# Kernel tuning notes

Measured on AMD Instinct MI355X. Metric: run time of the kernel, lower is better.

The kernel has to match this reference:

```python
import jax, jax.numpy as jnp
import numpy as np

B, N, CIN, COUT, R, K = 8, 4096, 64, 128, 32, 3
GROUPS = 8
GN_EPS = 1e-5


def setup_inputs() -> dict:
    key = jax.random.key(0)
    ks = jax.random.split(key, 6)
    w = lambda k, shape, fan: jax.random.normal(k, shape, jnp.float32) / np.sqrt(fan)
    return dict(
        features=jax.random.normal(ks[0], (B, CIN, N), jnp.float32),
        coords=jax.random.uniform(ks[1], (B, N, 3), jnp.float32),
        conv1_w=w(ks[2], (COUT, CIN, K, K, K), CIN * K ** 3), conv1_b=jnp.zeros((COUT,), jnp.float32),
        gn1_g=jnp.ones((COUT,), jnp.float32), gn1_b=jnp.zeros((COUT,), jnp.float32),
        conv2_w=w(ks[3], (COUT, COUT, K, K, K), COUT * K ** 3), conv2_b=jnp.zeros((COUT,), jnp.float32),
        gn2_g=jnp.ones((COUT,), jnp.float32), gn2_b=jnp.zeros((COUT,), jnp.float32),
        pt_w=w(ks[4], (COUT, CIN), CIN), pt_b=jnp.zeros((COUT,), jnp.float32),
        ptgn_g=jnp.ones((COUT,), jnp.float32), ptgn_b=jnp.zeros((COUT,), jnp.float32),
    )


def swish(x):
    return x * jax.nn.sigmoid(x)


def group_norm(x, gamma, beta):
    # x: [B, C, *spatial]
    b, c = x.shape[0], x.shape[1]
    sp = x.shape[2:]
    xg = x.reshape(b, GROUPS, -1)
    m = xg.mean(-1, keepdims=True)
    v = xg.var(-1, keepdims=True)
    xg = (xg - m) * jax.lax.rsqrt(v + GN_EPS)
    x = xg.reshape(b, c, *sp)
    shape = (1, c) + (1,) * len(sp)
    return x * gamma.reshape(shape) + beta.reshape(shape)


def conv3d(x, w, bias):
    p = K // 2
    y = jax.lax.conv_general_dilated(
        x, w, window_strides=(1, 1, 1), padding=[(p, p)] * 3,
        dimension_numbers=('NCDHW', 'OIDHW', 'NCDHW'))
    return y + bias[None, :, None, None, None]


def voxelize(features, coords):
    # PVCNN avg_voxelize: normalize coords to [0, R-1], round, scatter-mean.
    c = coords - coords.mean(axis=1, keepdims=True)          # [B,N,3]
    scale = 2.0 * jnp.linalg.norm(c, axis=-1).max(axis=1)     # [B], eps=0
    norm_coords = c / scale[:, None, None] + 0.5
    norm_coords = jnp.clip(norm_coords * R, 0.0, R - 1)       # float coords in [0, R-1]
    vox = jnp.round(norm_coords).astype(jnp.int32)
    flat = (vox[..., 0] * R + vox[..., 1]) * R + vox[..., 2]  # [B,N]
    seg = (flat + jnp.arange(B, dtype=jnp.int32)[:, None] * R ** 3).reshape(-1)
    ft = features.transpose(0, 2, 1).reshape(B * N, CIN)
    sums = jax.ops.segment_sum(ft, seg, num_segments=B * R ** 3)
    cnt = jax.ops.segment_sum(jnp.ones((B * N,), ft.dtype), seg, num_segments=B * R ** 3)
    grid = sums / jnp.maximum(cnt, 1.0)[:, None]
    grid = grid.reshape(B, R ** 3, CIN).transpose(0, 2, 1).reshape(B, CIN, R, R, R)
    return grid, norm_coords


def trilinear_devoxelize(grid, norm_coords):
    # grid: [B, C, R, R, R]; norm_coords: [B, N, 3] float in [0, R-1]
    c = grid.shape[1]
    f = jnp.floor(norm_coords)
    d = norm_coords - f                                       # frac, [B,N,3]
    f0 = f.astype(jnp.int32)
    f1 = jnp.minimum(f0 + 1, R - 1)
    gridf = grid.reshape(B, c, R ** 3)
    out = jnp.zeros((B, c, N), grid.dtype)
    for ix in (0, 1):
        for iy in (0, 1):
            for iz in (0, 1):
                xi = f1[..., 0] if ix else f0[..., 0]
                yi = f1[..., 1] if iy else f0[..., 1]
                zi = f1[..., 2] if iz else f0[..., 2]
                wx = d[..., 0] if ix else 1.0 - d[..., 0]
                wy = d[..., 1] if iy else 1.0 - d[..., 1]
                wz = d[..., 2] if iz else 1.0 - d[..., 2]
                idx = (xi * R + yi) * R + zi                  # [B,N]
                g = jnp.take_along_axis(gridf, idx[:, None, :], axis=2)  # [B,C,N]
                out = out + g * (wx * wy * wz)[:, None, :]
    return out


def reference(features, coords, conv1_w, conv1_b, gn1_g, gn1_b,
              conv2_w, conv2_b, gn2_g, gn2_b, pt_w, pt_b, ptgn_g, ptgn_b):
    grid, norm_coords = voxelize(features, coords)
    h = swish(group_norm(conv3d(grid, conv1_w, conv1_b), gn1_g, gn1_b))
    h = swish(group_norm(conv3d(h, conv2_w, conv2_b), gn2_g, gn2_b))
    devox = trilinear_devoxelize(h, norm_coords)              # [B, COUT, N]
    pf = jnp.einsum('oc,bcn->bon', pt_w, features) + pt_b[None, :, None]
    pf = swish(group_norm(pf, ptgn_g, ptgn_b))
    return devox + pf
```

## Files before the change

kernel.cpp:

```cpp
#include <hip/hip_runtime.h>
#include <hip/hip_bf16.h>
#include <cstdint>

#define B_ 8
#define N_ 4096
#define CIN_ 64
#define COUT_ 128
#define R_ 32
#define R3_ 32768
#define GROUPS_ 8
#define EPS_ 1e-5f

typedef float f32x4 __attribute__((ext_vector_type(4)));
typedef float f32x16 __attribute__((ext_vector_type(16)));
typedef __bf16 bf16x8 __attribute__((ext_vector_type(8)));
typedef unsigned short ushort8x __attribute__((ext_vector_type(8)));

static __device__ __forceinline__ unsigned short f2b(float f) {
    uint32_t u = __float_as_uint(f);
    uint32_t r = (u + 0x7fffu + ((u >> 16) & 1u)) >> 16;
    return (unsigned short)r;
}
static __device__ __forceinline__ float b2f(unsigned short u) {
    return __uint_as_float(((uint32_t)u) << 16);
}

__global__ void k_batch_stats(const float* __restrict__ coords, float* __restrict__ bstats) {
    int b = blockIdx.x;
    int tid = threadIdx.x;
    __shared__ float rb[256];
    __shared__ float smean[3];
    const float* cb = coords + (size_t)b * N_ * 3;
    float sx = 0.f, sy = 0.f, sz = 0.f;
    for (int n = tid; n < N_; n += 256) {
        sx += cb[n * 3 + 0];
        sy += cb[n * 3 + 1];
        sz += cb[n * 3 + 2];
    }
    float vals[3] = {sx, sy, sz};
    for (int k = 0; k < 3; ++k) {
        rb[tid] = vals[k];
        __syncthreads();
        for (int s = 128; s > 0; s >>= 1) {
            if (tid < s) rb[tid] += rb[tid + s];
            __syncthreads();
        }
        if (tid == 0) smean[k] = rb[0] / (float)N_;
        __syncthreads();
    }
    float mx = smean[0], my = smean[1], mz = smean[2];
    float m2 = 0.f;
    for (int n = tid; n < N_; n += 256) {
        float dx = cb[n * 3 + 0] - mx, dy = cb[n * 3 + 1] - my, dz = cb[n * 3 + 2] - mz;
        m2 = fmaxf(m2, dx * dx + dy * dy + dz * dz);
    }
    rb[tid] = m2;
    __syncthreads();
    for (int s = 128; s > 0; s >>= 1) {
        if (tid < s) rb[tid] = fmaxf(rb[tid], rb[tid + s]);
        __syncthreads();
    }
    if (tid == 0) {
        bstats[b * 4 + 0] = mx;
        bstats[b * 4 + 1] = my;
        bstats[b * 4 + 2] = mz;
        bstats[b * 4 + 3] = 2.0f * sqrtf(rb[0]);
    }
}

__global__ void k_points(const float* __restrict__ coords, const float* __restrict__ bstats,
                         float* __restrict__ ncoords, int* __restrict__ flatidx,
                         float* __restrict__ cnt) {
    int idx = blockIdx.x * 256 + threadIdx.x;
    int b = idx >> 12, n = idx & (N_ - 1);
    float scale = bstats[b * 4 + 3];
    int vi[3];
    for (int k = 0; k < 3; ++k) {
        float c = coords[((size_t)b * N_ + n) * 3 + k] - bstats[b * 4 + k];
        float nc = fminf(fmaxf((c / scale + 0.5f) * (float)R_, 0.0f), (float)(R_ - 1));
        ncoords[((size_t)b * N_ + n) * 3 + k] = nc;
        vi[k] = (int)rintf(nc);
    }
    int flat = (vi[0] * R_ + vi[1]) * R_ + vi[2];
    flatidx[idx] = flat;
    atomicAdd(&cnt[(size_t)b * R3_ + flat], 1.0f);
}

__global__ void k_scatter(const float* __restrict__ feat, const int* __restrict__ flatidx,
                          float* __restrict__ vox, int b0) {
    int bid = blockIdx.x;
    int nch = bid & 15, ci = (bid >> 4) & 63, bl = bid >> 10;
    int b = b0 + bl;
    int n = nch * 256 + threadIdx.x;
    float v = feat[((size_t)b * CIN_ + ci) * N_ + n];
    int flat = flatidx[b * N_ + n];
    atomicAdd(&vox[((size_t)bl * R3_ + flat) * CIN_ + ci], v);
}

__global__ void k_divide(const float* __restrict__ vox, const float* __restrict__ cnt,
                         unsigned short* __restrict__ gA, int b0) {
    size_t idx8 = (size_t)blockIdx.x * 256 + threadIdx.x;
    size_t voxel = idx8 >> 3;
    float c = cnt[(size_t)b0 * R3_ + voxel];
    float s = 1.0f / fmaxf(c, 1.0f);
    const float4* v4 = (const float4*)vox;
    float4 a = v4[idx8 * 2], b = v4[idx8 * 2 + 1];
    ushort8x o;
    o[0] = f2b(a.x * s); o[1] = f2b(a.y * s); o[2] = f2b(a.z * s); o[3] = f2b(a.w * s);
    o[4] = f2b(b.x * s); o[5] = f2b(b.y * s); o[6] = f2b(b.z * s); o[7] = f2b(b.w * s);
    ((ushort8x*)gA)[idx8] = o;
}

__global__ void k_feat2b(const float* __restrict__ f, unsigned short* __restrict__ fb, int b0) {
    size_t i8 = (size_t)blockIdx.x * 256 + threadIdx.x;
    const float4* s = (const float4*)(f + (size_t)b0 * CIN_ * N_);
    float4 a = s[i8 * 2], b = s[i8 * 2 + 1];
    ushort8x o;
    o[0] = f2b(a.x); o[1] = f2b(a.y); o[2] = f2b(a.z); o[3] = f2b(a.w);
    o[4] = f2b(b.x); o[5] = f2b(b.y); o[6] = f2b(b.z); o[7] = f2b(b.w);
    ((ushort8x*)fb)[i8] = o;
}

__global__ void k_wpack16(const float* __restrict__ w, unsigned short* __restrict__ wp,
                          int Cin, int taps) {
    int e = blockIdx.x * 256 + threadIdx.x;
    int total = taps * Cin * 128;
    if (e >= total) return;
    int KC = Cin / 32;
    int j = e & 7;
    int l = (e >> 3) & 63;
    int rest = e >> 9;
    int ct = rest & 7;
    int stepk = rest >> 3;
    int kc = stepk % KC;
    int t = stepk / KC;
    int co = ct * 16 + (l & 15);
    int ci = kc * 32 + (l >> 4) * 8 + j;
    wp[e] = f2b(w[((size_t)co * Cin + ci) * taps + t]);
}

__global__ void k_wpack32(const float* __restrict__ w, unsigned short* __restrict__ wp,
                          int Cin, int taps) {
    int e = blockIdx.x * 256 + threadIdx.x;
    int total = taps * Cin * 128;
    if (e >= total) return;
    int K16C = Cin / 16;
    int j = e & 7;
    int l = (e >> 3) & 63;
    int nt = (e >> 9) & 3;
    int sk = e >> 11;
    int k16 = sk % K16C;
    int t = sk / K16C;
    int co = nt * 32 + (l & 31);
    int ci = k16 * 16 + (l >> 5) * 8 + j;
    wp[e] = f2b(w[((size_t)co * Cin + ci) * taps + t]);
}

template <int CIN, bool FUSEGN>
__global__ __launch_bounds__(256) void k_conv32(
    const unsigned short* __restrict__ in, const unsigned short* __restrict__ wp,
    const float* __restrict__ bias, const float* __restrict__ instats,
    const float* __restrict__ ingamma, const float* __restrict__ inbeta,
    unsigned short* __restrict__ out, float* __restrict__ stats, int b0) {
    constexpr int K16C = CIN / 16;
    constexpr int S = CIN + 8;
    __shared__ unsigned short abuf[6 * 34 * S];
    __shared__ float s_sum[8], s_sq[8];
    __shared__ float sA[128], sB[128];
    int tid = threadIdx.x;
    int bid = blockIdx.x;
    int yg = bid & 7, x = (bid >> 3) & 31, bl = bid >> 8;
    int y0 = yg * 4;
    int lane = tid & 63, wv = tid >> 6;
    int yp = wv & 1, ch = wv >> 1;
    int col = lane & 31, kh = lane >> 5;

    if (tid < 8) { s_sum[tid] = 0.f; s_sq[tid] = 0.f; }
    if (FUSEGN && tid < 128) {
        int b = b0 + bl;
        int grp = tid >> 4;
        const float ic = 1.0f / (16.0f * R3_);
        float mean = instats[(b * 8 + grp) * 2 + 0] * ic;
        float var = instats[(b * 8 + grp) * 2 + 1] * ic - mean * mean;
        float inv = rsqrtf(var + EPS_);
        float A = ingamma[tid] * inv;
        sA[tid] = A;
        sB[tid] = inbeta[tid] - mean * A;
    }
    for (int i = tid; i < 6 * 2 * (CIN / 8); i += 256) {
        int cy = i / (2 * (CIN / 8));
        int r = i - cy * (2 * (CIN / 8));
        int hz = (r >= (CIN / 8)) ? 33 : 0;
        int c8 = r % (CIN / 8);
        ushort8x zz = {0, 0, 0, 0, 0, 0, 0, 0};
        *(ushort8x*)&abuf[(cy * 34 + hz) * S + c8 * 8] = zz;
    }

    float bv[2];
#pragma unroll
    for (int ntl = 0; ntl < 2; ++ntl) bv[ntl] = bias[ch * 64 + ntl * 32 + col];
    f32x16 acc[2][2];
#pragma unroll
    for (int my = 0; my < 2; ++my)
#pragma unroll
        for (int ntl = 0; ntl < 2; ++ntl)
#pragma unroll
            for (int r = 0; r < 16; ++r) acc[my][ntl][r] = bv[ntl];

    for (int xxi = 0; xxi < 3; ++xxi) {
        int xx = x + xxi - 1;
        if (xx < 0 || xx >= 32) continue;
        __syncthreads();
        for (int i = tid; i < 6 * 32 * (CIN / 8); i += 256) {
            int cy = i / (32 * (CIN / 8));
            int r = i - cy * (32 * (CIN / 8));
            int z = r / (CIN / 8), c8 = r - z * (CIN / 8);
            int yy = y0 - 1 + cy;
            ushort8x v = {0, 0, 0, 0, 0, 0, 0, 0};
            if (yy >= 0 && yy < 32) {
                v = *(const ushort8x*)&in[((size_t)bl * R3_ + xx * 1024 + yy * 32 + z) * CIN + c8 * 8];
                if (FUSEGN) {
#pragma unroll
                    for (int k = 0; k < 8; ++k) {
                        float xv = b2f(v[k]);
                        float s = sA[c8 * 8 + k] * xv + sB[c8 * 8 + k];
                        v[k] = f2b(s / (1.0f + expf(-s)));
                    }
                }
            }
            *(ushort8x*)&abuf[(cy * 34 + z + 1) * S + c8 * 8] = v;
        }
        __syncthreads();

        for (int dy = 0; dy < 3; ++dy) {
            for (int dz = 0; dz < 3; ++dz) {
                int t = (xxi * 3 + dy) * 3 + dz;
#pragma unroll
                for (int k16 = 0; k16 < K16C; ++k16) {
                    const unsigned short* wbase =
                        wp + ((size_t)((t * K16C + k16) * 4 + ch * 2) * 64 + lane) * 8;
                    bf16x8 b0f = *(const bf16x8*)wbase;
                    bf16x8 b1f = *(const bf16x8*)(wbase + 512);
#pragma unroll
                    for (int my = 0; my < 2; ++my) {
                        int cy = yp * 2 + my + dy;
                        bf16x8 a = *(const bf16x8*)
                            &abuf[(cy * 34 + col + dz) * S + k16 * 16 + kh * 8];
                        acc[my][0] = __builtin_amdgcn_mfma_f32_32x32x16_bf16(a, b0f, acc[my][0], 0, 0, 0);
                        acc[my][1] = __builtin_amdgcn_mfma_f32_32x32x16_bf16(a, b1f, acc[my][1], 0, 0, 0);
                    }
                }
            }
        }
    }

    float lsum[2] = {0.f, 0.f}, lsq[2] = {0.f, 0.f};
#pragma unroll
    for (int my = 0; my < 2; ++my) {
        int y = y0 + yp * 2 + my;
#pragma unroll
        for (int ntl = 0; ntl < 2; ++ntl) {
            int co = ch * 64 + ntl * 32 + col;
            unsigned short* op = out + ((size_t)bl * R3_ + x * 1024 + y * 32) * 128 + co;
#pragma unroll
            for (int r = 0; r < 16; ++r) {
                int z = (r & 3) + 8 * (r >> 2) + 4 * kh;
                float vv = acc[my][ntl][r];
                op[(size_t)z * 128] = f2b(vv);
                lsum[ntl] += vv;
                lsq[ntl] += vv * vv;
            }
        }
    }
#pragma unroll
    for (int ntl = 0; ntl < 2; ++ntl) {
        float s = lsum[ntl], q = lsq[ntl];
        s += __shfl_xor(s, 32); q += __shfl_xor(q, 32);
        s += __shfl_xor(s, 1);  q += __shfl_xor(q, 1);
        s += __shfl_xor(s, 2);  q += __shfl_xor(q, 2);
        s += __shfl_xor(s, 4);  q += __shfl_xor(q, 4);
        s += __shfl_xor(s, 8);  q += __shfl_xor(q, 8);
        if (lane == 0 || lane == 16) {
            int g = ch * 4 + ntl * 2 + (col >> 4);
            atomicAdd(&s_sum[g], s);
            atomicAdd(&s_sq[g], q);
        }
    }
    __syncthreads();
    if (tid < 8) {
        int b = b0 + bl;
        atomicAdd(&stats[((size_t)b * 8 + tid) * 2 + 0], s_sum[tid]);
        atomicAdd(&stats[((size_t)b * 8 + tid) * 2 + 1], s_sq[tid]);
    }
}

__global__ __launch_bounds__(256) void k_point_mfma(
    const unsigned short* __restrict__ featb, const unsigned short* __restrict__ wp,
    const float* __restrict__ bias, unsigned short* __restrict__ pf,
    float* __restrict__ stats, int b0) {
    __shared__ __align__(16) unsigned short ALds[256 * 72];
    int tid = threadIdx.x;
    int bid = blockIdx.x;
    int bl = bid >> 4;
    int n0 = (bid & 15) * 256;
    int b = b0 + bl;
    int lane = tid & 63, wv = tid >> 6;
    int nh = wv & 1, ch = wv >> 1;
    int mrow = lane & 15, quad = lane >> 4;

    {
        int c0 = (tid >> 5) * 8;
        int nl = tid & 31;
        for (int u = 0; u < 8; ++u) {
            int n = u * 32 + nl;
            ushort8x v;
#pragma unroll
            for (int k = 0; k < 8; ++k)
                v[k] = featb[((size_t)(bl * 64 + c0 + k)) * N_ + n0 + n];
            *(ushort8x*)&ALds[n * 72 + c0] = v;
        }
    }

    bf16x8 bfr[2][4];
#pragma unroll
    for (int kc = 0; kc < 2; ++kc)
#pragma unroll
        for (int ct = 0; ct < 4; ++ct)
            bfr[kc][ct] = *(const bf16x8*)&wp[((size_t)((kc * 8) + ch * 4 + ct) * 64 + lane) * 8];

    float bv[4];
#pragma unroll
    for (int ct = 0; ct < 4; ++ct) bv[ct] = bias[ch * 64 + ct * 16 + mrow];
    f32x4 acc[8][4];
#pragma unroll
    for (int mt = 0; mt < 8; ++mt)
#pragma unroll
        for (int ct = 0; ct < 4; ++ct) {
            acc[mt][ct][0] = bv[ct]; acc[mt][ct][1] = bv[ct];
            acc[mt][ct][2] = bv[ct]; acc[mt][ct][3] = bv[ct];
        }

    __syncthreads();
#pragma unroll
    for (int kc = 0; kc < 2; ++kc) {
#pragma unroll
        for (int mt = 0; mt < 8; ++mt) {
            bf16x8 a = *(const bf16x8*)
                &ALds[(nh * 128 + mt * 16 + mrow) * 72 + kc * 32 + quad * 8];
#pragma unroll
            for (int ct = 0; ct < 4; ++ct)
                acc[mt][ct] = __builtin_amdgcn_mfma_f32_16x16x32_bf16(
                    a, bfr[kc][ct], acc[mt][ct], 0, 0, 0);
        }
    }

#pragma unroll
    for (int ct = 0; ct < 4; ++ct) {
        int co = ch * 64 + ct * 16 + mrow;
        float s = 0.f, q = 0.f;
#pragma unroll
        for (int mt = 0; mt < 8; ++mt) {
#pragma unroll
            for (int r = 0; r < 4; ++r) {
                int n = nh * 128 + mt * 16 + quad * 4 + r;
                float vv = acc[mt][ct][r];
                pf[((size_t)bl * N_ + n0 + n) * 128 + co] = f2b(vv);
                s += vv;
                q += vv * vv;
            }
        }
#pragma unroll
        for (int off = 32; off >= 1; off >>= 1) {
            s += __shfl_xor(s, off);
            q += __shfl_xor(q, off);
        }
        if (lane == 0) {
            int g = ch * 4 + ct;
            atomicAdd(&stats[((size_t)b * 8 + g) * 2 + 0], s);
            atomicAdd(&stats[((size_t)b * 8 + g) * 2 + 1], q);
        }
    }
}

__global__ __launch_bounds__(256) void k_final(
    const unsigned short* __restrict__ grid, const float* __restrict__ ncoords,
    const unsigned short* __restrict__ pf,
    const float* __restrict__ stats2, const float* __restrict__ g2g,
    const float* __restrict__ g2b,
    const float* __restrict__ statsPt, const float* __restrict__ pgg,
    const float* __restrict__ pgb,
    float* __restrict__ out, int b0) {
    __shared__ int sidx[32][8];
    __shared__ float swt[32][8];
    __shared__ float devt[32 * 129];
    int bid = blockIdx.x;
    int bl = bid >> 7;
    int b = b0 + bl;
    int n0 = (bid & 127) * 32;
    int tid = threadIdx.x;
    if (tid < 32) {
        int n = n0 + tid;
        const float* nc = ncoords + ((size_t)b * N_ + n) * 3;
        float fc[3] = {nc[0], nc[1], nc[2]};
        int i0[3], i1[3];
        float dd[3];
        for (int k = 0; k < 3; ++k) {
            float fl = floorf(fc[k]);
            i0[k] = (int)fl;
            i1[k] = min(i0[k] + 1, R_ - 1);
            dd[k] = fc[k] - fl;
        }
#pragma unroll
        for (int k = 0; k < 8; ++k) {
            int ix = (k >> 2) & 1, iy = (k >> 1) & 1, iz = k & 1;
            int xi = ix ? i1[0] : i0[0];
            int yi = iy ? i1[1] : i0[1];
            int zi = iz ? i1[2] : i0[2];
            sidx[tid][k] = (xi * R_ + yi) * R_ + zi;
            float wx = ix ? dd[0] : 1.0f - dd[0];
            float wy = iy ? dd[1] : 1.0f - dd[1];
            float wz = iz ? dd[2] : 1.0f - dd[2];
            swt[tid][k] = wx * wy * wz;
        }
    }
    __syncthreads();
    int co = tid & 127, pg = tid >> 7;
    int grp = co >> 4;
    const float ic2 = 1.0f / (16.0f * R3_);
    float mean2 = stats2[(b * 8 + grp) * 2 + 0] * ic2;
    float var2 = stats2[(b * 8 + grp) * 2 + 1] * ic2 - mean2 * mean2;
    float inv2 = rsqrtf(var2 + EPS_);
    float A2 = g2g[co] * inv2, B2 = g2b[co] - mean2 * A2;
    const float icp = 1.0f / (16.0f * N_);
    float meanp = statsPt[(b * 8 + grp) * 2 + 0] * icp;
    float varp = statsPt[(b * 8 + grp) * 2 + 1] * icp - meanp * meanp;
    float invp = rsqrtf(varp + EPS_);
    float Ap = pgg[co] * invp, Bp = pgb[co] - meanp * Ap;

    const unsigned short* gp = grid + (size_t)bl * R3_ * 128 + co;
    for (int p = pg; p < 32; p += 2) {
        float acc = 0.f;
#pragma unroll
        for (int k = 0; k < 8; ++k) {
            float s = A2 * b2f(gp[(size_t)sidx[p][k] * 128]) + B2;
            acc += swt[p][k] * (s / (1.0f + expf(-s)));
        }
        float xv = b2f(pf[((size_t)bl * N_ + n0 + p) * 128 + co]);
        float s = Ap * xv + Bp;
        devt[p * 129 + co] = acc + s / (1.0f + expf(-s));
    }
    __syncthreads();
    int pp = tid & 31, cg = tid >> 5;
    float* op = out + (size_t)b * 128 * N_ + n0 + pp;
    for (int c = cg * 16; c < cg * 16 + 16; ++c)
        op[(size_t)c * N_] = devt[pp * 129 + c];
}

extern "C" void kernel_launch(void* const* d_in, const int* in_sizes, int n_in,
                              void* d_out, int out_size, void* d_ws, size_t ws_size,
                              hipStream_t stream) {
    const float* features = (const float*)d_in[0];
    const float* coords = (const float*)d_in[1];
    const float* c1w = (const float*)d_in[2];
    const float* c1b = (const float*)d_in[3];
    const float* g1g = (const float*)d_in[4];
    const float* g1b = (const float*)d_in[5];
    const float* c2w = (const float*)d_in[6];
    const float* c2b = (const float*)d_in[7];
    const float* g2g = (const float*)d_in[8];
    const float* g2b = (const float*)d_in[9];
    const float* ptw = (const float*)d_in[10];
    const float* ptb = (const float*)d_in[11];
    const float* pgg = (const float*)d_in[12];
    const float* pgb = (const float*)d_in[13];
    float* outp = (float*)d_out;

    size_t globals = ((size_t)B_ * R3_ * 4 + 255 & ~(size_t)255)
                   + ((size_t)B_ * N_ * 3 * 4 + 255 & ~(size_t)255)
                   + ((size_t)B_ * N_ * 4 + 255 & ~(size_t)255)
                   + 256 + 2048
                   + ((size_t)27 * 64 * 128 * 2 + 255 & ~(size_t)255)
                   + ((size_t)27 * 128 * 128 * 2 + 255 & ~(size_t)255)
                   + ((size_t)64 * 128 * 2 + 255 & ~(size_t)255)
                   + 8192;
    int CB = 1;
    for (int cb = 8; cb >= 1; cb >>= 1) {
        size_t need = globals
                    + ((size_t)cb * R3_ * 64 * 4)
                    + ((size_t)cb * R3_ * 64 * 2)
                    + ((size_t)cb * R3_ * 128 * 2)
                    + ((size_t)cb * N_ * 128 * 2)
                    + ((size_t)cb * 64 * N_ * 2);
        if (need <= ws_size) { CB = cb; break; }
    }

    char* ws = (char*)d_ws;
    size_t o = 0;
    auto alloc = [&](size_t bytes) {
        size_t r = o;
        o += (bytes + 255) & ~(size_t)255;
        return r;
    };
    float* voxC = (float*)(ws + alloc((size_t)CB * R3_ * 64 * 4));
    unsigned short* gC = (unsigned short*)voxC;
    unsigned short* gA = (unsigned short*)(ws + alloc((size_t)CB * R3_ * 64 * 2));
    unsigned short* gB = (unsigned short*)(ws + alloc((size_t)CB * R3_ * 128 * 2));
    unsigned short* pfbuf = (unsigned short*)(ws + alloc((size_t)CB * N_ * 128 * 2));
    unsigned short* featbc = (unsigned short*)(ws + alloc((size_t)CB * 64 * N_ * 2));
    float* cnt = (float*)(ws + alloc((size_t)B_ * R3_ * 4));
    float* ncoords = (float*)(ws + alloc((size_t)B_ * N_ * 3 * 4));
    int* flatidx = (int*)(ws + alloc((size_t)B_ * N_ * 4));
    float* bstats = (float*)(ws + alloc(256));
    float* statsAll = (float*)(ws + alloc(2048));
    float* stats1 = statsAll;
    float* stats2 = statsAll + 128;
    float* statsPt = statsAll + 256;
    unsigned short* wp1 = (unsigned short*)(ws + alloc((size_t)27 * 64 * 128 * 2));
    unsigned short* wp2 = (unsigned short*)(ws + alloc((size_t)27 * 128 * 128 * 2));
    unsigned short* wpPt = (unsigned short*)(ws + alloc((size_t)64 * 128 * 2));

    hipMemsetAsync(cnt, 0, (size_t)B_ * R3_ * 4, stream);
    hipMemsetAsync(statsAll, 0, 1536, stream);
    k_wpack32<<<(27 * 64 * 128 + 255) / 256, 256, 0, stream>>>(c1w, wp1, 64, 27);
    k_wpack32<<<(27 * 128 * 128 + 255) / 256, 256, 0, stream>>>(c2w, wp2, 128, 27);
    k_wpack16<<<(64 * 128 + 255) / 256, 256, 0, stream>>>(ptw, wpPt, 64, 1);
    k_batch_stats<<<B_, 256, 0, stream>>>(coords, bstats);
    k_points<<<B_ * N_ / 256, 256, 0, stream>>>(coords, bstats, ncoords, flatidx, cnt);

    for (int b0 = 0; b0 < B_; b0 += CB) {
        hipMemsetAsync(voxC, 0, (size_t)CB * R3_ * 64 * 4, stream);
        k_feat2b<<<CB * 128, 256, 0, stream>>>(features, featbc, b0);
        k_scatter<<<CB * 64 * 16, 256, 0, stream>>>(features, flatidx, voxC, b0);
        k_divide<<<CB * 1024, 256, 0, stream>>>(voxC, cnt, gA, b0);
        k_conv32<64, false><<<CB * 256, 256, 0, stream>>>(
            gA, wp1, c1b, nullptr, nullptr, nullptr, gB, stats1, b0);
        k_conv32<128, true><<<CB * 256, 256, 0, stream>>>(
            gB, wp2, c2b, stats1, g1g, g1b, gC, stats2, b0);
        k_point_mfma<<<CB * 16, 256, 0, stream>>>(featbc, wpPt, ptb, pfbuf, statsPt, b0);
        k_final<<<CB * 128, 256, 0, stream>>>(gC, ncoords, pfbuf,
                                              stats2, g2g, g2b, statsPt, pgg, pgb, outp, b0);
    }
}
```

Before: 746.7 us.

## Remap conv warps to one y-row each with all 128 output channels; use fast swish

After: 823.2 us. +10.2%, slower.

```diff
diff --git a/kernel.cpp b/kernel.cpp
--- a/kernel.cpp
+++ b/kernel.cpp
@@ -23,6 +23,9 @@
 }
 static __device__ __forceinline__ float b2f(unsigned short u) {
     return __uint_as_float(((uint32_t)u) << 16);
+}
+static __device__ __forceinline__ float fswish(float s) {
+    return s * __builtin_amdgcn_rcpf(1.0f + __expf(-s));
 }
 
 __global__ void k_batch_stats(const float* __restrict__ coords, float* __restrict__ bstats) {
@@ -166,13 +169,12 @@
     constexpr int S = CIN + 8;
     __shared__ unsigned short abuf[6 * 34 * S];
     __shared__ float s_sum[8], s_sq[8];
-    __shared__ float sA[128], sB[128];
+    __shared__ __align__(16) float sA[128], sB[128];
     int tid = threadIdx.x;
     int bid = blockIdx.x;
     int yg = bid & 7, x = (bid >> 3) & 31, bl = bid >> 8;
     int y0 = yg * 4;
     int lane = tid & 63, wv = tid >> 6;
-    int yp = wv & 1, ch = wv >> 1;
     int col = lane & 31, kh = lane >> 5;
 
     if (tid < 8) { s_sum[tid] = 0.f; s_sq[tid] = 0.f; }
@@ -196,16 +198,14 @@
         *(ushort8x*)&abuf[(cy * 34 + hz) * S + c8 * 8] = zz;
     }
 
-    float bv[2];
-#pragma unroll
-    for (int ntl = 0; ntl < 2; ++ntl) bv[ntl] = bias[ch * 64 + ntl * 32 + col];
-    f32x16 acc[2][2];
-#pragma unroll
-    for (int my = 0; my < 2; ++my)
-#pragma unroll
-        for (int ntl = 0; ntl < 2; ++ntl)
-#pragma unroll
-            for (int r = 0; r < 16; ++r) acc[my][ntl][r] = bv[ntl];
+    float bv[4];
+#pragma unroll
+    for (int nt = 0; nt < 4; ++nt) bv[nt] = bias[nt * 32 + col];
+    f32x16 acc[4];
+#pragma unroll
+    for (int nt = 0; nt < 4; ++nt)
+#pragma unroll
+        for (int r = 0; r < 16; ++r) acc[nt][r] = bv[nt];
 
     for (int xxi = 0; xxi < 3; ++xxi) {
         int xx = x + xxi - 1;
@@ -220,12 +220,18 @@
             if (yy >= 0 && yy < 32) {
                 v = *(const ushort8x*)&in[((size_t)bl * R3_ + xx * 1024 + yy * 32 + z) * CIN + c8 * 8];
                 if (FUSEGN) {
-#pragma unroll
-                    for (int k = 0; k < 8; ++k) {
-                        float xv = b2f(v[k]);
-                        float s = sA[c8 * 8 + k] * xv + sB[c8 * 8 + k];
-                        v[k] = f2b(s / (1.0f + expf(-s)));
-                    }
+                    float4 A0 = *(const float4*)&sA[c8 * 8];
+                    float4 A1 = *(const float4*)&sA[c8 * 8 + 4];
+                    float4 B0 = *(const float4*)&sB[c8 * 8];
+                    float4 B1 = *(const float4*)&sB[c8 * 8 + 4];
+                    v[0] = f2b(fswish(A0.x * b2f(v[0]) + B0.x));
+                    v[1] = f2b(fswish(A0.y * b2f(v[1]) + B0.y));
+                    v[2] = f2b(fswish(A0.z * b2f(v[2]) + B0.z));
+                    v[3] = f2b(fswish(A0.w * b2f(v[3]) + B0.w));
+                    v[4] = f2b(fswish(A1.x * b2f(v[4]) + B1.x));
+                    v[5] = f2b(fswish(A1.y * b2f(v[5]) + B1.y));
+                    v[6] = f2b(fswish(A1.z * b2f(v[6]) + B1.z));
+                    v[7] = f2b(fswish(A1.w * b2f(v[7]) + B1.w));
                 }
             }
             *(ushort8x*)&abuf[(cy * 34 + z + 1) * S + c8 * 8] = v;
@@ -233,55 +239,53 @@
         __syncthreads();
 
         for (int dy = 0; dy < 3; ++dy) {
+            int cy = wv + dy;
             for (int dz = 0; dz < 3; ++dz) {
                 int t = (xxi * 3 + dy) * 3 + dz;
 #pragma unroll
                 for (int k16 = 0; k16 < K16C; ++k16) {
+                    bf16x8 a = *(const bf16x8*)
+                        &abuf[(cy * 34 + col + dz) * S + k16 * 16 + kh * 8];
                     const unsigned short* wbase =
-                        wp + ((size_t)((t * K16C + k16) * 4 + ch * 2) * 64 + lane) * 8;
-                    bf16x8 b0f = *(const bf16x8*)wbase;
-                    bf16x8 b1f = *(const bf16x8*)(wbase + 512);
-#pragma unroll
-                    for (int my = 0; my < 2; ++my) {
-                        int cy = yp * 2 + my + dy;
-                        bf16x8 a = *(const bf16x8*)
-                            &abuf[(cy * 34 + col + dz) * S + k16 * 16 + kh * 8];
-                        acc[my][0] = __builtin_amdgcn_mfma_f32_32x32x16_bf16(a, b0f, acc[my][0], 0, 0, 0);
-                        acc[my][1] = __builtin_amdgcn_mfma_f32_32x32x16_bf16(a, b1f, acc[my][1], 0, 0, 0);
-                    }
+                        wp + ((size_t)((t * K16C + k16) * 4) * 64 + lane) * 8;
+                    acc[0] = __builtin_amdgcn_mfma_f32_32x32x16_bf16(
+                        a, *(const bf16x8*)(wbase + 0 * 512), acc[0], 0, 0, 0);
+                    acc[1] = __builtin_amdgcn_mfma_f32_32x32x16_bf16(
+                        a, *(const bf16x8*)(wbase + 1 * 512), acc[1], 0, 0, 0);
+                    acc[2] = __builtin_amdgcn_mfma_f32_32x32x16_bf16(
+                        a, *(const bf16x8*)(wbase + 2 * 512), acc[2], 0, 0, 0);
+                    acc[3] = __builtin_amdgcn_mfma_f32_32x32x16_bf16(
+                        a, *(const bf16x8*)(wbase + 3 * 512), acc[3], 0, 0, 0);
                 }
             }
         }
     }
 
-    float lsum[2] = {0.f, 0.f}, lsq[2] = {0.f, 0.f};
-#pragma unroll
-    for (int my = 0; my < 2; ++my) {
-        int y = y0 + yp * 2 + my;
-#pragma unroll
-        for (int ntl = 0; ntl < 2; ++ntl) {
-            int co = ch * 64 + ntl * 32 + col;
-            unsigned short* op = out + ((size_t)bl * R3_ + x * 1024 + y * 32) * 128 + co;
-#pragma unroll
-            for (int r = 0; r < 16; ++r) {
-                int z = (r & 3) + 8 * (r >> 2) + 4 * kh;
-                float vv = acc[my][ntl][r];
-                op[(size_t)z * 128] = f2b(vv);
-                lsum[ntl] += vv;
-                lsq[ntl] += vv * vv;
-            }
-        }
-    }
-#pragma unroll
-    for (int ntl = 0; ntl < 2; ++ntl) {
-        float s = lsum[ntl], q = lsq[ntl];
+    int y = y0 + wv;
+    unsigned short* obase = out + ((size_t)bl * R3_ + x * 1024 + y * 32) * 128;
+    float lsum[4] = {0.f, 0.f, 0.f, 0.f}, lsq[4] = {0.f, 0.f, 0.f, 0.f};
+#pragma unroll
+    for (int nt = 0; nt < 4; ++nt) {
+        int co = nt * 32 + col;
+#pragma unroll
+        for (int r = 0; r < 16; ++r) {
+            int z = (r & 3) + 8 * (r >> 2) + 4 * kh;
+            float vv = acc[nt][r];
+            obase[(size_t)z * 128 + co] = f2b(vv);
+            lsum[nt] += vv;
+            lsq[nt] += vv * vv;
+        }
+    }
+#pragma unroll
+    for (int nt = 0; nt < 4; ++nt) {
+        float s = lsum[nt], q = lsq[nt];
         s += __shfl_xor(s, 32); q += __shfl_xor(q, 32);
         s += __shfl_xor(s, 1);  q += __shfl_xor(q, 1);
         s += __shfl_xor(s, 2);  q += __shfl_xor(q, 2);
         s += __shfl_xor(s, 4);  q += __shfl_xor(q, 4);
         s += __shfl_xor(s, 8);  q += __shfl_xor(q, 8);
         if (lane == 0 || lane == 16) {
-            int g = ch * 4 + ntl * 2 + (col >> 4);
+            int g = nt * 2 + (col >> 4);
             atomicAdd(&s_sum[g], s);
             atomicAdd(&s_sq[g], q);
         }
@@ -443,11 +447,10 @@
 #pragma unroll
         for (int k = 0; k < 8; ++k) {
             float s = A2 * b2f(gp[(size_t)sidx[p][k] * 128]) + B2;
-            acc += swt[p][k] * (s / (1.0f + expf(-s)));
+            acc += swt[p][k] * fswish(s);
         }
         float xv = b2f(pf[((size_t)bl * N_ + n0 + p) * 128 + co]);
-        float s = Ap * xv + Bp;
-        devt[p * 129 + co] = acc + s / (1.0f + expf(-s));
+        devt[p * 129 + co] = acc + fswish(Ap * xv + Bp);
     }
     __syncthreads();
     int pp = tid & 31, cg = tid >> 5;
```

## Split GroupNorm+swish out of conv2 staging and fold bf16 feature conversion

Applied to the files above, without the earlier changes.

Measured after the change: 666.2 us. 10.8% less time.

```diff
diff --git a/kernel.cpp b/kernel.cpp
--- a/kernel.cpp
+++ b/kernel.cpp
@@ -24,15 +24,18 @@
 static __device__ __forceinline__ float b2f(unsigned short u) {
     return __uint_as_float(((uint32_t)u) << 16);
 }
+static __device__ __forceinline__ float fswish(float s) {
+    return s * __builtin_amdgcn_rcpf(1.0f + __expf(-s));
+}
 
 __global__ void k_batch_stats(const float* __restrict__ coords, float* __restrict__ bstats) {
     int b = blockIdx.x;
     int tid = threadIdx.x;
-    __shared__ float rb[256];
+    __shared__ float rb[1024];
     __shared__ float smean[3];
     const float* cb = coords + (size_t)b * N_ * 3;
     float sx = 0.f, sy = 0.f, sz = 0.f;
-    for (int n = tid; n < N_; n += 256) {
+    for (int n = tid; n < N_; n += 1024) {
         sx += cb[n * 3 + 0];
         sy += cb[n * 3 + 1];
         sz += cb[n * 3 + 2];
@@ -41,7 +44,7 @@
     for (int k = 0; k < 3; ++k) {
         rb[tid] = vals[k];
         __syncthreads();
-        for (int s = 128; s > 0; s >>= 1) {
+        for (int s = 512; s > 0; s >>= 1) {
             if (tid < s) rb[tid] += rb[tid + s];
             __syncthreads();
         }
@@ -50,13 +53,13 @@
     }
     float mx = smean[0], my = smean[1], mz = smean[2];
     float m2 = 0.f;
-    for (int n = tid; n < N_; n += 256) {
+    for (int n = tid; n < N_; n += 1024) {
         float dx = cb[n * 3 + 0] - mx, dy = cb[n * 3 + 1] - my, dz = cb[n * 3 + 2] - mz;
         m2 = fmaxf(m2, dx * dx + dy * dy + dz * dz);
     }
     rb[tid] = m2;
     __syncthreads();
-    for (int s = 128; s > 0; s >>= 1) {
+    for (int s = 512; s > 0; s >>= 1) {
         if (tid < s) rb[tid] = fmaxf(rb[tid], rb[tid + s]);
         __syncthreads();
     }
@@ -109,16 +112,6 @@
     o[0] = f2b(a.x * s); o[1] = f2b(a.y * s); o[2] = f2b(a.z * s); o[3] = f2b(a.w * s);
     o[4] = f2b(b.x * s); o[5] = f2b(b.y * s); o[6] = f2b(b.z * s); o[7] = f2b(b.w * s);
     ((ushort8x*)gA)[idx8] = o;
-}
-
-__global__ void k_feat2b(const float* __restrict__ f, unsigned short* __restrict__ fb, int b0) {
-    size_t i8 = (size_t)blockIdx.x * 256 + threadIdx.x;
-    const float4* s = (const float4*)(f + (size_t)b0 * CIN_ * N_);
-    float4 a = s[i8 * 2], b = s[i8 * 2 + 1];
-    ushort8x o;
-    o[0] = f2b(a.x); o[1] = f2b(a.y); o[2] = f2b(a.z); o[3] = f2b(a.w);
-    o[4] = f2b(b.x); o[5] = f2b(b.y); o[6] = f2b(b.z); o[7] = f2b(b.w);
-    ((ushort8x*)fb)[i8] = o;
 }
 
 __global__ void k_wpack16(const float* __restrict__ w, unsigned short* __restrict__ wp,
@@ -144,29 +137,49 @@
     int e = blockIdx.x * 256 + threadIdx.x;
     int total = taps * Cin * 128;
     if (e >= total) return;
-    int K16C = Cin / 16;
+    int K16 = Cin / 16;
     int j = e & 7;
     int l = (e >> 3) & 63;
     int nt = (e >> 9) & 3;
     int sk = e >> 11;
-    int k16 = sk % K16C;
-    int t = sk / K16C;
+    int k16 = sk % K16;
+    int t = sk / K16;
     int co = nt * 32 + (l & 31);
     int ci = k16 * 16 + (l >> 5) * 8 + j;
     wp[e] = f2b(w[((size_t)co * Cin + ci) * taps + t]);
 }
 
-template <int CIN, bool FUSEGN>
-__global__ __launch_bounds__(256) void k_conv32(
+__global__ void k_gnswish(unsigned short* __restrict__ g, const float* __restrict__ stats,
+                          const float* __restrict__ gamma, const float* __restrict__ beta,
+                          int b0) {
+    size_t idx8 = (size_t)blockIdx.x * 256 + threadIdx.x;
+    int c0 = (int)(idx8 & 15) * 8;
+    int b = b0 + (int)(idx8 >> 19);
+    int grp = c0 >> 4;
+    const float cntv = 16.0f * R3_;
+    float mean = stats[(b * 8 + grp) * 2 + 0] / cntv;
+    float var = stats[(b * 8 + grp) * 2 + 1] / cntv - mean * mean;
+    float inv = rsqrtf(var + EPS_);
+    ushort8x v = ((ushort8x*)g)[idx8];
+#pragma unroll
+    for (int k = 0; k < 8; ++k) {
+        float A = gamma[c0 + k] * inv;
+        float Bc = beta[c0 + k] - mean * A;
+        v[k] = f2b(fswish(A * b2f(v[k]) + Bc));
+    }
+    ((ushort8x*)g)[idx8] = v;
+}
+
+template <int CIN>
+__global__ __launch_bounds__(256) void k_conv(
     const unsigned short* __restrict__ in, const unsigned short* __restrict__ wp,
-    const float* __restrict__ bias, const float* __restrict__ instats,
-    const float* __restrict__ ingamma, const float* __restrict__ inbeta,
-    unsigned short* __restrict__ out, float* __restrict__ stats, int b0) {
-    constexpr int K16C = CIN / 16;
+    const float* __restrict__ bias, unsigned short* __restrict__ out,
+    float* __restrict__ stats, int b0) {
+    constexpr int K16 = CIN / 16;
     constexpr int S = CIN + 8;
-    __shared__ unsigned short abuf[6 * 34 * S];
+    constexpr int ZP = 6 * 32 * S;
+    __shared__ __align__(16) unsigned short abuf[(6 * 32 + 1) * S];
     __shared__ float s_sum[8], s_sq[8];
-    __shared__ float sA[128], sB[128];
     int tid = threadIdx.x;
     int bid = blockIdx.x;
     int yg = bid & 7, x = (bid >> 3) & 31, bl = bid >> 8;
@@ -176,24 +189,9 @@
     int col = lane & 31, kh = lane >> 5;
 
     if (tid < 8) { s_sum[tid] = 0.f; s_sq[tid] = 0.f; }
-    if (FUSEGN && tid < 128) {
-        int b = b0 + bl;
-        int grp = tid >> 4;
-        const float ic = 1.0f / (16.0f * R3_);
-        float mean = instats[(b * 8 + grp) * 2 + 0] * ic;
-        float var = instats[(b * 8 + grp) * 2 + 1] * ic - mean * mean;
-        float inv = rsqrtf(var + EPS_);
-        float A = ingamma[tid] * inv;
-        sA[tid] = A;
-        sB[tid] = inbeta[tid] - mean * A;
-    }
-    for (int i = tid; i < 6 * 2 * (CIN / 8); i += 256) {
-        int cy = i / (2 * (CIN / 8));
-        int r = i - cy * (2 * (CIN / 8));
-        int hz = (r >= (CIN / 8)) ? 33 : 0;
-        int c8 = r % (CIN / 8);
+    for (int i = tid; i < S / 8; i += 256) {
         ushort8x zz = {0, 0, 0, 0, 0, 0, 0, 0};
-        *(ushort8x*)&abuf[(cy * 34 + hz) * S + c8 * 8] = zz;
+        *(ushort8x*)&abuf[ZP + i * 8] = zz;
     }
 
     float bv[2];
@@ -217,40 +215,36 @@
             int z = r / (CIN / 8), c8 = r - z * (CIN / 8);
             int yy = y0 - 1 + cy;
             ushort8x v = {0, 0, 0, 0, 0, 0, 0, 0};
-            if (yy >= 0 && yy < 32) {
+            if (yy >= 0 && yy < 32)
                 v = *(const ushort8x*)&in[((size_t)bl * R3_ + xx * 1024 + yy * 32 + z) * CIN + c8 * 8];
-                if (FUSEGN) {
-#pragma unroll
-                    for (int k = 0; k < 8; ++k) {
-                        float xv = b2f(v[k]);
-                        float s = sA[c8 * 8 + k] * xv + sB[c8 * 8 + k];
-                        v[k] = f2b(s / (1.0f + expf(-s)));
+            *(ushort8x*)&abuf[(cy * 32 + z) * S + c8 * 8] = v;
+        }
+        __syncthreads();
+
+        for (int dy = 0; dy < 3; ++dy) {
+            for (int dz = 0; dz < 3; ++dz) {
+                int t = (xxi * 3 + dy) * 3 + dz;
+                int z = col + dz - 1;
+                bool zok = (z >= 0 && z < 32);
+#pragma unroll
+                for (int k16 = 0; k16 < K16; ++k16) {
+                    const unsigned short* wbase =
+                        wp + ((size_t)((t * K16 + k16) * 4 + ch * 2) * 64 + lane) * 8;
+                    bf16x8 b0f = *(const bf16x8*)wbase;
+                    bf16x8 b1f = *(const bf16x8*)(wbase + 512);
+#pragma unroll
+                    for (int my = 0; my < 2; ++my) {
+                        int cy = yp * 2 + my + dy;
+                        int off = zok ? (cy * 32 + z) * S + k16 * 16 + kh * 8
+                                      : ZP + k16 * 16 + kh * 8;
+                        bf16x8 a = *(const bf16x8*)&abuf[off];
+                        acc[my][0] = __builtin_amdgcn_mfma_f32_32x32x16_bf16(
+                            a, b0f, acc[my][0], 0, 0, 0);
+                        acc[my][1] = __builtin_amdgcn_mfma_f32_32x32x16_bf16(
+                            a, b1f, acc[my][1], 0, 0, 0);
                     }
                 }
             }
-            *(ushort8x*)&abuf[(cy * 34 + z + 1) * S + c8 * 8] = v;
-        }
-        __syncthreads();
-
-        for (int dy = 0; dy < 3; ++dy) {
-            for (int dz = 0; dz < 3; ++dz) {
-                int t = (xxi * 3 + dy) * 3 + dz;
-#pragma unroll
-                for (int k16 = 0; k16 < K16C; ++k16) {
-                    const unsigned short* wbase =
-                        wp + ((size_t)((t * K16C + k16) * 4 + ch * 2) * 64 + lane) * 8;
-                    bf16x8 b0f = *(const bf16x8*)wbase;
-                    bf16x8 b1f = *(const bf16x8*)(wbase + 512);
-#pragma unroll
-                    for (int my = 0; my < 2; ++my) {
-                        int cy = yp * 2 + my + dy;
-                        bf16x8 a = *(const bf16x8*)
-                            &abuf[(cy * 34 + col + dz) * S + k16 * 16 + kh * 8];
-                        acc[my][0] = __builtin_amdgcn_mfma_f32_32x32x16_bf16(a, b0f, acc[my][0], 0, 0, 0);
-                        acc[my][1] = __builtin_amdgcn_mfma_f32_32x32x16_bf16(a, b1f, acc[my][1], 0, 0, 0);
-                    }
-                }
-            }
         }
     }
 
@@ -258,15 +252,15 @@
 #pragma unroll
     for (int my = 0; my < 2; ++my) {
         int y = y0 + yp * 2 + my;
+        unsigned short* obase = out + ((size_t)bl * R3_ + x * 1024 + y * 32) * 128;
 #pragma unroll
         for (int ntl = 0; ntl < 2; ++ntl) {
             int co = ch * 64 + ntl * 32 + col;
-            unsigned short* op = out + ((size_t)bl * R3_ + x * 1024 + y * 32) * 128 + co;
 #pragma unroll
             for (int r = 0; r < 16; ++r) {
                 int z = (r & 3) + 8 * (r >> 2) + 4 * kh;
                 float vv = acc[my][ntl][r];
-                op[(size_t)z * 128] = f2b(vv);
+                obase[(size_t)z * 128 + co] = f2b(vv);
                 lsum[ntl] += vv;
                 lsq[ntl] += vv * vv;
             }
@@ -295,7 +289,7 @@
 }
 
 __global__ __launch_bounds__(256) void k_point_mfma(
-    const unsigned short* __restrict__ featb, const unsigned short* __restrict__ wp,
+    const float* __restrict__ featf, const unsigned short* __restrict__ wp,
     const float* __restrict__ bias, unsigned short* __restrict__ pf,
     float* __restrict__ stats, int b0) {
     __shared__ __align__(16) unsigned short ALds[256 * 72];
@@ -316,7 +310,7 @@
             ushort8x v;
 #pragma unroll
             for (int k = 0; k < 8; ++k)
-                v[k] = featb[((size_t)(bl * 64 + c0 + k)) * N_ + n0 + n];
+                v[k] = f2b(featf[((size_t)(b * 64 + c0 + k)) * N_ + n0 + n]);
             *(ushort8x*)&ALds[n * 72 + c0] = v;
         }
     }
@@ -443,11 +437,10 @@
 #pragma unroll
         for (int k = 0; k < 8; ++k) {
             float s = A2 * b2f(gp[(size_t)sidx[p][k] * 128]) + B2;
-            acc += swt[p][k] * (s / (1.0f + expf(-s)));
+            acc += swt[p][k] * fswish(s);
         }
         float xv = b2f(pf[((size_t)bl * N_ + n0 + p) * 128 + co]);
-        float s = Ap * xv + Bp;
-        devt[p * 129 + co] = acc + s / (1.0f + expf(-s));
+        devt[p * 129 + co] = acc + fswish(Ap * xv + Bp);
     }
     __syncthreads();
     int pp = tid & 31, cg = tid >> 5;
@@ -489,8 +482,7 @@
                     + ((size_t)cb * R3_ * 64 * 4)
                     + ((size_t)cb * R3_ * 64 * 2)
                     + ((size_t)cb * R3_ * 128 * 2)
-                    + ((size_t)cb * N_ * 128 * 2)
-                    + ((size_t)cb * 64 * N_ * 2);
+                    + ((size_t)cb * N_ * 128 * 2);
         if (need <= ws_size) { CB = cb; break; }
     }
 
@@ -506,7 +498,6 @@
     unsigned short* gA = (unsigned short*)(ws + alloc((size_t)CB * R3_ * 64 * 2));
     unsigned short* gB = (unsigned short*)(ws + alloc((size_t)CB * R3_ * 128 * 2));
     unsigned short* pfbuf = (unsigned short*)(ws + alloc((size_t)CB * N_ * 128 * 2));
-    unsigned short* featbc = (unsigned short*)(ws + alloc((size_t)CB * 64 * N_ * 2));
     float* cnt = (float*)(ws + alloc((size_t)B_ * R3_ * 4));
     float* ncoords = (float*)(ws + alloc((size_t)B_ * N_ * 3 * 4));
     int* flatidx = (int*)(ws + alloc((size_t)B_ * N_ * 4));
@@ -524,19 +515,17 @@
     k_wpack32<<<(27 * 64 * 128 + 255) / 256, 256, 0, stream>>>(c1w, wp1, 64, 27);
     k_wpack32<<<(27 * 128 * 128 + 255) / 256, 256, 0, stream>>>(c2w, wp2, 128, 27);
     k_wpack16<<<(64 * 128 + 255) / 256, 256, 0, stream>>>(ptw, wpPt, 64, 1);
-    k_batch_stats<<<B_, 256, 0, stream>>>(coords, bstats);
+    k_batch_stats<<<B_, 1024, 0, stream>>>(coords, bstats);
     k_points<<<B_ * N_ / 256, 256, 0, stream>>>(coords, bstats, ncoords, flatidx, cnt);
 
     for (int b0 = 0; b0 < B_; b0 += CB) {
         hipMemsetAsync(voxC, 0, (size_t)CB * R3_ * 64 * 4, stream);
-        k_feat2b<<<CB * 128, 256, 0, stream>>>(features, featbc, b0);
         k_scatter<<<CB * 64 * 16, 256, 0, stream>>>(features, flatidx, voxC, b0);
         k_divide<<<CB * 1024, 256, 0, stream>>>(voxC, cnt, gA, b0);
-        k_conv32<64, false><<<CB * 256, 256, 0, stream>>>(
-            gA, wp1, c1b, nullptr, nullptr, nullptr, gB, stats1, b0);
-        k_conv32<128, true><<<CB * 256, 256, 0, stream>>>(
-            gB, wp2, c2b, stats1, g1g, g1b, gC, stats2, b0);
-        k_point_mfma<<<CB * 16, 256, 0, stream>>>(featbc, wpPt, ptb, pfbuf, statsPt, b0);
+        k_conv<64><<<CB * 256, 256, 0, stream>>>(gA, wp1, c1b, gB, stats1, b0);
+        k_gnswish<<<CB * 2048, 256, 0, stream>>>(gB, stats1, g1g, g1b, b0);
+        k_conv<128><<<CB * 256, 256, 0, stream>>>(gB, wp2, c2b, gC, stats2, b0);
+        k_point_mfma<<<CB * 16, 256, 0, stream>>>(features, wpPt, ptb, pfbuf, statsPt, b0);
         k_final<<<CB * 128, 256, 0, stream>>>(gC, ncoords, pfbuf,
                                               stats2, g2g, g2b, statsPt, pgg, pgb, outp, b0);
     }
```
